# Kernel tuning notes

Measured on AMD Instinct MI355X. Metric: run time of the kernel, lower is better.

## Reference

```python
import jax, jax.numpy as jnp
import numpy as np

B, C, H, W = 4, 512, 64, 64
CI = C // 2  # inter_channel


def setup_inputs() -> dict:
    key = jax.random.key(0)
    ks = jax.random.split(key, 5)
    x = jax.random.normal(ks[0], (B, C, H, W), dtype=jnp.float32)
    # 1x1 convs with bias=False == channel-mixing matrices (out_ch, in_ch)
    w_phi = jax.random.normal(ks[1], (CI, C), dtype=jnp.float32) * 0.02
    w_theta = jax.random.normal(ks[2], (CI, C), dtype=jnp.float32) * 0.02
    w_g = jax.random.normal(ks[3], (CI, C), dtype=jnp.float32) * 0.02
    w_mask = jax.random.normal(ks[4], (C, CI), dtype=jnp.float32) * 0.02
    return {"x": x, "w_phi": w_phi, "w_theta": w_theta, "w_g": w_g, "w_mask": w_mask}


def reference(x, w_phi, w_theta, w_g, w_mask):
    b, c, h, w = x.shape
    n = h * w
    ci = w_phi.shape[0]
    xf = x.reshape(b, c, n)  # (b, c, N)
    # 1x1 convs as channel matmuls -> (b, ci, N)
    phi = jnp.einsum('oc,bcn->bon', w_phi, xf)
    theta = jnp.einsum('oc,bcn->bon', w_theta, xf)
    g = jnp.einsum('oc,bcn->bon', w_g, xf)
    # f = theta^T @ phi : (b, N, N), unscaled scores
    f = jnp.einsum('bcn,bcm->bnm', theta, phi)
    a = jax.nn.softmax(f, axis=-1)
    # y = a @ g^T, produced directly in (b, ci, N) layout (fuses the permute)
    y = jnp.einsum('bnm,bcm->bcn', a, g)
    # conv_mask: 1x1 conv back to C channels
    out = jnp.einsum('oc,bcn->bon', w_mask, y)
    return out.reshape(b, c, h, w)
```

## Files before the change

kernel.cpp:

```cpp
#include <hip/hip_runtime.h>


#define BB 4
#define CC 512
#define NN_SP 4096
#define CI 256

typedef _Float16 f16x8 __attribute__((ext_vector_type(8)));
typedef float f32x4 __attribute__((ext_vector_type(4)));

__device__ __forceinline__ void async16(const void* gsrc, void* ldst) {
  __builtin_amdgcn_global_load_lds(
      (const __attribute__((address_space(1))) unsigned int*)gsrc,
      (__attribute__((address_space(3))) unsigned int*)ldst, 16, 0, 0);
}

__global__ __launch_bounds__(256) void convert_w(
    const float* __restrict__ wphi, const float* __restrict__ wtheta,
    const float* __restrict__ wg, const float* __restrict__ wmask,
    _Float16* __restrict__ wpt, _Float16* __restrict__ wgh, _Float16* __restrict__ wmh) {
  int i = blockIdx.x * 256 + threadIdx.x;
  if (i < 512 * 512) {
    int row = i >> 9, k = i & 511;
    float v = (row < 256) ? wphi[row * 512 + k] : wtheta[(row - 256) * 512 + k];
    wpt[i] = (_Float16)v;
  } else if (i < 512 * 512 + 256 * 512) {
    int j = i - 512 * 512;
    wgh[j] = (_Float16)wg[j];
  } else {
    int j = i - 512 * 512 - 256 * 512;
    wmh[j] = (_Float16)wmask[j];
  }
}

__global__ __launch_bounds__(256) void transpose_x(const float* __restrict__ x,
                                                   _Float16* __restrict__ xT) {
  __shared__ float tile[64][65];
  const int n0 = blockIdx.x * 64, c0 = blockIdx.y * 64, b = blockIdx.z;
  const int tx = threadIdx.x & 63, ty = threadIdx.x >> 6;
  const float* xb = x + (long long)b * CC * NN_SP;
#pragma unroll
  for (int i = 0; i < 16; ++i) {
    int row = i * 4 + ty;
    tile[row][tx] = xb[(long long)(c0 + row) * NN_SP + n0 + tx];
  }
  __syncthreads();
  _Float16* xTb = xT + (long long)b * NN_SP * CC;
#pragma unroll
  for (int i = 0; i < 16; ++i) {
    int row = i * 4 + ty;
    xTb[(long long)(n0 + row) * CC + c0 + tx] = (_Float16)tile[tx][row];
  }
}

template <int M, int NT, int K, bool F16OUT>
__global__ __launch_bounds__(256, 2) void gemm_bt(
    const _Float16* __restrict__ Ab, const _Float16* __restrict__ Btb,
    void* __restrict__ Cb, long long sA, long long sB, long long sC) {
  __shared__ _Float16 As[128 * 32];
  __shared__ _Float16 Bs[128 * 32];
  const int tid = threadIdx.x, lane = tid & 63, w = tid >> 6;
  const int wm = w >> 1, wn = w & 1;
  const int l15 = lane & 15, lq = lane >> 4;
  const int b = blockIdx.z;
  const _Float16* A = Ab + (long long)b * sA;
  const _Float16* Bt = Btb + (long long)b * sB;
  const int m0 = blockIdx.y * 128, n0 = blockIdx.x * 128;

  f32x4 acc[4][4];
#pragma unroll
  for (int i = 0; i < 4; ++i)
#pragma unroll
    for (int j = 0; j < 4; ++j) acc[i][j] = (f32x4){0.f, 0.f, 0.f, 0.f};

  for (int k0 = 0; k0 < K; k0 += 32) {
    __syncthreads();
#pragma unroll
    for (int j = 0; j < 2; ++j) {
      int chw = j * 256 + w * 64;
      int ch = chw + lane;
      int row = ch >> 2, kc = ch & 3;
      async16(A + (long long)(m0 + row) * K + k0 + kc * 8, (void*)(As + chw * 8));
      async16(Bt + (long long)(n0 + row) * K + k0 + kc * 8, (void*)(Bs + chw * 8));
    }
    __syncthreads();
    f16x8 af[4], bf[4];
#pragma unroll
    for (int mt = 0; mt < 4; ++mt)
      af[mt] = *(const f16x8*)(As + (wm * 64 + mt * 16 + l15) * 32 + lq * 8);
#pragma unroll
    for (int nt = 0; nt < 4; ++nt)
      bf[nt] = *(const f16x8*)(Bs + (wn * 64 + nt * 16 + l15) * 32 + lq * 8);
#pragma unroll
    for (int mt = 0; mt < 4; ++mt)
#pragma unroll
      for (int nt = 0; nt < 4; ++nt)
        acc[mt][nt] = __builtin_amdgcn_mfma_f32_16x16x32_f16(af[mt], bf[nt], acc[mt][nt], 0, 0, 0);
  }

#pragma unroll
  for (int mt = 0; mt < 4; ++mt)
#pragma unroll
    for (int nt = 0; nt < 4; ++nt)
#pragma unroll
      for (int r = 0; r < 4; ++r) {
        int row = m0 + wm * 64 + mt * 16 + lq * 4 + r;
        int col = n0 + wn * 64 + nt * 16 + l15;
        if (F16OUT)
          ((_Float16*)Cb + (long long)b * sC)[(long long)row * NT + col] = (_Float16)acc[mt][nt][r];
        else
          ((float*)Cb + (long long)b * sC)[(long long)row * NT + col] = acc[mt][nt][r];
      }
}

__global__ __launch_bounds__(512, 2) void flash_attn3(
    const _Float16* __restrict__ pt, const _Float16* __restrict__ g,
    _Float16* __restrict__ yT) {
  __shared__ _Float16 Stg[2][2][16384];
  __shared__ _Float16 Ps[8][2048];
  const int tid = threadIdx.x, lane = tid & 63, w = tid >> 6;
  const int hw = w >> 2, wp = w & 3;
  const int l15 = lane & 15, lq = lane >> 4;

  const int idx = blockIdx.x;
  const int b = (idx >> 1) & 3;
  const int q0 = (((idx >> 3) << 1) | (idx & 1)) * 64;
  const int kvbase = hw * 2048;
  const _Float16* __restrict__ ptb = pt + (long long)b * NN_SP * 512;
  const _Float16* __restrict__ gb = g + (long long)b * CI * NN_SP;

  int offPhi[4], offG[4], chw_[4];
#pragma unroll
  for (int j = 0; j < 4; ++j) {
    int u = wp * 256 + j * 64 + lane;
    chw_[j] = wp * 256 + j * 64;
    int us = u ^ ((u >> 3) & 7);
    int k2 = us >> 9, nv8 = (us >> 6) & 7, r15 = (us >> 2) & 15, rq = us & 3;
    offPhi[j] = (nv8 * 16 + r15) * 512 + k2 * 32 + rq * 8;
    int kq = us >> 8, ct4 = (us >> 6) & 3;
    offG[j] = (ct4 * 16 + r15) * 4096 + kq * 32 + rq * 8;
  }
  const int rswz = (l15 * 4 + lq) ^ ((l15 >> 1) & 7);

  f16x8 qreg[8];
#pragma unroll
  for (int kk = 0; kk < 8; ++kk)
    qreg[kk] = *(const f16x8*)(
        ptb + (long long)(q0 + wp * 16 + l15) * 512 + 256 + kk * 32 + lq * 8);

  f32x4 yacc[16];
#pragma unroll
  for (int nt = 0; nt < 16; ++nt) yacc[nt] = (f32x4){0.f, 0.f, 0.f, 0.f};
  float mrow[4] = {-3e38f, -3e38f, -3e38f, -3e38f};
  float lrow[4] = {0.f, 0.f, 0.f, 0.f};

  auto issue = [&](int mq, int bi) {
    if (mq >= 64) return;
    int t = mq >> 2, mp = mq & 3, kv0 = kvbase + t * 128;
#pragma unroll
    for (int hh = 0; hh < 2; ++hh) {
      int sub = mp * 2 + hh;
      _Float16* buf = Stg[hw][bi] + hh * 8192;
      if (sub < 4) {
        const _Float16* basep = ptb + (long long)kv0 * 512 + sub * 64;
#pragma unroll
        for (int j = 0; j < 4; ++j)
          async16(basep + offPhi[j], (void*)(buf + chw_[j] * 8));
      } else {
        const _Float16* baseg = gb + (long long)(sub - 4) * 64 * 4096 + kv0;
#pragma unroll
        for (int j = 0; j < 4; ++j)
          async16(baseg + offG[j], (void*)(buf + chw_[j] * 8));
      }
    }
  };

  int p = 0;
  issue(0, 0);

  for (int t = 0; t < 16; ++t) {
    f32x4 S[8];
#pragma unroll
    for (int i = 0; i < 8; ++i) S[i] = (f32x4){0.f, 0.f, 0.f, 0.f};

#pragma unroll
    for (int mp = 0; mp < 2; ++mp) {
      asm volatile("s_waitcnt vmcnt(0)" ::: "memory");
      asm volatile("s_barrier" ::: "memory");
      issue(p + 1, (p + 1) & 1);
      const _Float16* bufb = Stg[hw][p & 1];
      __builtin_amdgcn_s_setprio(1);
#pragma unroll
      for (int hh = 0; hh < 2; ++hh) {
        int c = mp * 2 + hh;
        const _Float16* buf = bufb + hh * 8192;
#pragma unroll
        for (int k2 = 0; k2 < 2; ++k2)
#pragma unroll
          for (int nv = 0; nv < 8; ++nv) {
            f16x8 bf = *(const f16x8*)(buf + (k2 * 512 + nv * 64 + rswz) * 8);
            S[nv] = __builtin_amdgcn_mfma_f32_16x16x32_f16(qreg[c * 2 + k2], bf, S[nv], 0, 0, 0);
          }
      }
      __builtin_amdgcn_s_setprio(0);
      ++p;
    }

    float alpha[4];
#pragma unroll
    for (int r = 0; r < 4; ++r) {
      float mx = fmaxf(fmaxf(S[0][r], S[1][r]), fmaxf(S[2][r], S[3][r]));
      mx = fmaxf(mx, fmaxf(fmaxf(S[4][r], S[5][r]), fmaxf(S[6][r], S[7][r])));
#pragma unroll
      for (int d = 1; d < 16; d <<= 1) mx = fmaxf(mx, __shfl_xor(mx, d, 64));
      float nm = fmaxf(mrow[r], mx);
      alpha[r] = __expf(mrow[r] - nm);
      mrow[r] = nm;
      float ps = 0.f;
#pragma unroll
      for (int nv = 0; nv < 8; ++nv) {
        float pv = __expf(S[nv][r] - nm);
        S[nv][r] = pv;
        ps += pv;
      }
#pragma unroll
      for (int d = 1; d < 16; d <<= 1) ps += __shfl_xor(ps, d, 64);
      lrow[r] = lrow[r] * alpha[r] + ps;
    }
    {
      f32x4 al = {alpha[0], alpha[1], alpha[2], alpha[3]};
#pragma unroll
      for (int nt = 0; nt < 16; ++nt) yacc[nt] *= al;
    }

#pragma unroll
    for (int nv = 0; nv < 8; ++nv) {
      int kq = nv >> 1;
      int lqr = (nv & 1) * 2 + (l15 >> 3);
      int e = l15 & 7;
#pragma unroll
      for (int r = 0; r < 4; ++r) {
        int u = kq * 64 + lqr * 16 + lq * 4 + r;
        int us = u ^ ((u >> 3) & 7);
        Ps[w][us * 8 + e] = (_Float16)S[nv][r];
      }
    }
    f16x8 aP[4];
#pragma unroll
    for (int kq = 0; kq < 4; ++kq) {
      int ur = kq * 64 + lane;
      int urs = ur ^ ((ur >> 3) & 7);
      aP[kq] = *(const f16x8*)(&Ps[w][urs * 8]);
    }

#pragma unroll
    for (int mp = 0; mp < 2; ++mp) {
      if (t == 15 && mp == 1) {
        asm volatile("s_waitcnt vmcnt(0)" ::: "memory");
      } else {
        asm volatile("s_waitcnt vmcnt(0)" ::: "memory");
      }
      asm volatile("s_barrier" ::: "memory");
      issue(p + 1, (p + 1) & 1);
      const _Float16* bufb = Stg[hw][p & 1];
      __builtin_amdgcn_s_setprio(1);
#pragma unroll
      for (int hh = 0; hh < 2; ++hh) {
        int cg = mp * 2 + hh;
        const _Float16* buf = bufb + hh * 8192;
#pragma unroll
        for (int kq = 0; kq < 4; ++kq)
#pragma unroll
          for (int ct = 0; ct < 4; ++ct) {
            f16x8 bf = *(const f16x8*)(buf + (kq * 256 + ct * 64 + rswz) * 8);
            yacc[cg * 4 + ct] =
                __builtin_amdgcn_mfma_f32_16x16x32_f16(aP[kq], bf, yacc[cg * 4 + ct], 0, 0, 0);
          }
      }
      __builtin_amdgcn_s_setprio(0);
      ++p;
    }
  }

  __syncthreads();
  float* mbuf = (float*)Stg;
  float* sbuf = (float*)((char*)Stg + 81920);
  if (hw == 1) {
#pragma unroll
    for (int r = 0; r < 4; ++r) {
      int rr = wp * 16 + lq * 4 + r;
#pragma unroll
      for (int nt = 0; nt < 16; ++nt)
        mbuf[rr * 257 + nt * 16 + l15] = yacc[nt][r];
      if (l15 == 0) {
        sbuf[rr * 2 + 0] = mrow[r];
        sbuf[rr * 2 + 1] = lrow[r];
      }
    }
  }
  __syncthreads();
  if (hw == 0) {
    _Float16* yTb = yT + (long long)b * NN_SP * CI;
#pragma unroll
    for (int r = 0; r < 4; ++r) {
      int rr = wp * 16 + lq * 4 + r;
      float m2 = sbuf[rr * 2 + 0], l2 = sbuf[rr * 2 + 1];
      float m = fmaxf(mrow[r], m2);
      float w1 = __expf(mrow[r] - m), w2 = __expf(m2 - m);
      float inv = 1.f / (w1 * lrow[r] + w2 * l2);
      int row = q0 + rr;
#pragma unroll
      for (int nt = 0; nt < 16; ++nt) {
        float v2 = mbuf[rr * 257 + nt * 16 + l15];
        yTb[(long long)row * CI + nt * 16 + l15] =
            (_Float16)((w1 * yacc[nt][r] + w2 * v2) * inv);
      }
    }
  }
}

extern "C" void kernel_launch(void* const* d_in, const int* in_sizes, int n_in,
                              void* d_out, int out_size, void* d_ws, size_t ws_size,
                              hipStream_t stream) {
  const float* x = (const float*)d_in[0];
  const float* w_phi = (const float*)d_in[1];
  const float* w_theta = (const float*)d_in[2];
  const float* w_g = (const float*)d_in[3];
  const float* w_mask = (const float*)d_in[4];
  float* out = (float*)d_out;
  char* ws = (char*)d_ws;

  _Float16* xT = (_Float16*)(ws);
  _Float16* pt = (_Float16*)(ws + 16777216);
  _Float16* gB = (_Float16*)(ws + 33554432);
  _Float16* yT = (_Float16*)(ws + 41943040);
  _Float16* wpt = (_Float16*)(ws + 50331648);
  _Float16* wg = (_Float16*)(ws + 50855936);
  _Float16* wm = (_Float16*)(ws + 51118080);

  convert_w<<<2048, 256, 0, stream>>>(w_phi, w_theta, w_g, w_mask, wpt, wg, wm);
  transpose_x<<<dim3(64, 8, 4), 256, 0, stream>>>(x, xT);
  gemm_bt<4096, 512, 512, true><<<dim3(4, 32, 4), 256, 0, stream>>>(
      xT, wpt, pt, 4096LL * 512, 0, 4096LL * 512);
  gemm_bt<256, 4096, 512, true><<<dim3(32, 2, 4), 256, 0, stream>>>(
      wg, xT, gB, 0, 4096LL * 512, 256LL * 4096);
  flash_attn3<<<dim3(256), 512, 0, stream>>>(pt, gB, yT);
  gemm_bt<512, 4096, 256, false><<<dim3(32, 4, 4), 256, 0, stream>>>(
      wm, yT, out, 0, 4096LL * 256, 512LL * 4096);
}
```

Before: 252.1 us.

## Widen GEMM K-tile with swizzled LDS, vectorize transpose, compute row sums via MFMA

New measurement: 240.7 us. -4.5%, faster.

```diff
diff --git a/kernel.cpp b/kernel.cpp
--- a/kernel.cpp
+++ b/kernel.cpp
@@ -45,11 +45,16 @@
     tile[row][tx] = xb[(long long)(c0 + row) * NN_SP + n0 + tx];
   }
   __syncthreads();
+  const int cx = threadIdx.x & 31;
+  const int ny = threadIdx.x >> 5;
   _Float16* xTb = xT + (long long)b * NN_SP * CC;
 #pragma unroll
-  for (int i = 0; i < 16; ++i) {
-    int row = i * 4 + ty;
-    xTb[(long long)(n0 + row) * CC + c0 + tx] = (_Float16)tile[tx][row];
+  for (int i = 0; i < 8; ++i) {
+    int n = i * 8 + ny;
+    union { _Float16 h[2]; unsigned int u; } pk;
+    pk.h[0] = (_Float16)tile[cx * 2][n];
+    pk.h[1] = (_Float16)tile[cx * 2 + 1][n];
+    *(unsigned int*)(xTb + (long long)(n0 + n) * CC + c0 + cx * 2) = pk.u;
   }
 }
 
@@ -57,8 +62,8 @@
 __global__ __launch_bounds__(256, 2) void gemm_bt(
     const _Float16* __restrict__ Ab, const _Float16* __restrict__ Btb,
     void* __restrict__ Cb, long long sA, long long sB, long long sC) {
-  __shared__ _Float16 As[128 * 32];
-  __shared__ _Float16 Bs[128 * 32];
+  __shared__ _Float16 As[128 * 64];
+  __shared__ _Float16 Bs[128 * 64];
   const int tid = threadIdx.x, lane = tid & 63, w = tid >> 6;
   const int wm = w >> 1, wn = w & 1;
   const int l15 = lane & 15, lq = lane >> 4;
@@ -73,29 +78,37 @@
 #pragma unroll
     for (int j = 0; j < 4; ++j) acc[i][j] = (f32x4){0.f, 0.f, 0.f, 0.f};
 
-  for (int k0 = 0; k0 < K; k0 += 32) {
+  for (int k0 = 0; k0 < K; k0 += 64) {
     __syncthreads();
 #pragma unroll
-    for (int j = 0; j < 2; ++j) {
+    for (int j = 0; j < 4; ++j) {
       int chw = j * 256 + w * 64;
       int ch = chw + lane;
-      int row = ch >> 2, kc = ch & 3;
+      int us = ch ^ ((ch >> 3) & 7);
+      int row = us >> 3, kc = us & 7;
       async16(A + (long long)(m0 + row) * K + k0 + kc * 8, (void*)(As + chw * 8));
       async16(Bt + (long long)(n0 + row) * K + k0 + kc * 8, (void*)(Bs + chw * 8));
     }
     __syncthreads();
-    f16x8 af[4], bf[4];
-#pragma unroll
-    for (int mt = 0; mt < 4; ++mt)
-      af[mt] = *(const f16x8*)(As + (wm * 64 + mt * 16 + l15) * 32 + lq * 8);
-#pragma unroll
-    for (int nt = 0; nt < 4; ++nt)
-      bf[nt] = *(const f16x8*)(Bs + (wn * 64 + nt * 16 + l15) * 32 + lq * 8);
-#pragma unroll
-    for (int mt = 0; mt < 4; ++mt)
-#pragma unroll
-      for (int nt = 0; nt < 4; ++nt)
-        acc[mt][nt] = __builtin_amdgcn_mfma_f32_16x16x32_f16(af[mt], bf[nt], acc[mt][nt], 0, 0, 0);
+#pragma unroll
+    for (int kh = 0; kh < 2; ++kh) {
+      f16x8 af[4], bf[4];
+#pragma unroll
+      for (int mt = 0; mt < 4; ++mt) {
+        int c = (wm * 64 + mt * 16 + l15) * 8 + kh * 4 + lq;
+        af[mt] = *(const f16x8*)(As + (c ^ ((c >> 3) & 7)) * 8);
+      }
+#pragma unroll
+      for (int nt = 0; nt < 4; ++nt) {
+        int c = (wn * 64 + nt * 16 + l15) * 8 + kh * 4 + lq;
+        bf[nt] = *(const f16x8*)(Bs + (c ^ ((c >> 3) & 7)) * 8);
+      }
+#pragma unroll
+      for (int mt = 0; mt < 4; ++mt)
+#pragma unroll
+        for (int nt = 0; nt < 4; ++nt)
+          acc[mt][nt] = __builtin_amdgcn_mfma_f32_16x16x32_f16(af[mt], bf[nt], acc[mt][nt], 0, 0, 0);
+    }
   }
 
 #pragma unroll
@@ -148,11 +161,15 @@
     qreg[kk] = *(const f16x8*)(
         ptb + (long long)(q0 + wp * 16 + l15) * 512 + 256 + kk * 32 + lq * 8);
 
+  f16x8 onesf;
+#pragma unroll
+  for (int j = 0; j < 8; ++j) onesf[j] = (_Float16)1.f;
+
   f32x4 yacc[16];
 #pragma unroll
   for (int nt = 0; nt < 16; ++nt) yacc[nt] = (f32x4){0.f, 0.f, 0.f, 0.f};
+  f32x4 lacc = (f32x4){0.f, 0.f, 0.f, 0.f};
   float mrow[4] = {-3e38f, -3e38f, -3e38f, -3e38f};
-  float lrow[4] = {0.f, 0.f, 0.f, 0.f};
 
   auto issue = [&](int mq, int bi) {
     if (mq >= 64) return;
@@ -206,32 +223,32 @@
       ++p;
     }
 
-    float alpha[4];
+    float nm[4];
+    int grew = 0;
 #pragma unroll
     for (int r = 0; r < 4; ++r) {
       float mx = fmaxf(fmaxf(S[0][r], S[1][r]), fmaxf(S[2][r], S[3][r]));
       mx = fmaxf(mx, fmaxf(fmaxf(S[4][r], S[5][r]), fmaxf(S[6][r], S[7][r])));
 #pragma unroll
       for (int d = 1; d < 16; d <<= 1) mx = fmaxf(mx, __shfl_xor(mx, d, 64));
-      float nm = fmaxf(mrow[r], mx);
-      alpha[r] = __expf(mrow[r] - nm);
-      mrow[r] = nm;
-      float ps = 0.f;
-#pragma unroll
-      for (int nv = 0; nv < 8; ++nv) {
-        float pv = __expf(S[nv][r] - nm);
-        S[nv][r] = pv;
-        ps += pv;
-      }
-#pragma unroll
-      for (int d = 1; d < 16; d <<= 1) ps += __shfl_xor(ps, d, 64);
-      lrow[r] = lrow[r] * alpha[r] + ps;
-    }
-    {
-      f32x4 al = {alpha[0], alpha[1], alpha[2], alpha[3]};
+      nm[r] = fmaxf(mrow[r], mx);
+      grew |= (mx > mrow[r]);
+    }
+    if (__ballot(grew)) {
+      f32x4 al;
+#pragma unroll
+      for (int r = 0; r < 4; ++r) {
+        al[r] = __expf(mrow[r] - nm[r]);
+        mrow[r] = nm[r];
+      }
 #pragma unroll
       for (int nt = 0; nt < 16; ++nt) yacc[nt] *= al;
-    }
+      lacc *= al;
+    }
+#pragma unroll
+    for (int r = 0; r < 4; ++r)
+#pragma unroll
+      for (int nv = 0; nv < 8; ++nv) S[nv][r] = __expf(S[nv][r] - mrow[r]);
 
 #pragma unroll
     for (int nv = 0; nv < 8; ++nv) {
@@ -254,12 +271,12 @@
     }
 
 #pragma unroll
+    for (int kq = 0; kq < 4; ++kq)
+      lacc = __builtin_amdgcn_mfma_f32_16x16x32_f16(aP[kq], onesf, lacc, 0, 0, 0);
+
+#pragma unroll
     for (int mp = 0; mp < 2; ++mp) {
-      if (t == 15 && mp == 1) {
-        asm volatile("s_waitcnt vmcnt(0)" ::: "memory");
-      } else {
-        asm volatile("s_waitcnt vmcnt(0)" ::: "memory");
-      }
+      asm volatile("s_waitcnt vmcnt(0)" ::: "memory");
       asm volatile("s_barrier" ::: "memory");
       issue(p + 1, (p + 1) & 1);
       const _Float16* bufb = Stg[hw][p & 1];
@@ -294,7 +311,7 @@
         mbuf[rr * 257 + nt * 16 + l15] = yacc[nt][r];
       if (l15 == 0) {
         sbuf[rr * 2 + 0] = mrow[r];
-        sbuf[rr * 2 + 1] = lrow[r];
+        sbuf[rr * 2 + 1] = lacc[r];
       }
     }
   }
@@ -307,7 +324,7 @@
       float m2 = sbuf[rr * 2 + 0], l2 = sbuf[rr * 2 + 1];
       float m = fmaxf(mrow[r], m2);
       float w1 = __expf(mrow[r] - m), w2 = __expf(m2 - m);
-      float inv = 1.f / (w1 * lrow[r] + w2 * l2);
+      float inv = 1.f / (w1 * lacc[r] + w2 * l2);
       int row = q0 + rr;
 #pragma unroll
       for (int nt = 0; nt < 16; ++nt) {
```
